# Performance work log

Measured on AMD Instinct MI355X. Metric: run time of the kernel, lower is better.

The kernel has to match this reference:

```python
import jax, jax.numpy as jnp
import numpy as np

EPS = 1e-10


def setup_inputs() -> dict:
    key = jax.random.key(0)
    k1, k2 = jax.random.split(key)
    x = jax.random.normal(k1, (64, 512, 256), dtype=jnp.float32)          # (N, code_dim, T)
    codebooks = jax.random.normal(k2, (6, 1024, 512), dtype=jnp.float32)  # (Q, nb_code, code_dim)
    return {"x": x, "codebooks": codebooks}


def _quantize_layer(x_flat, cb):
    # x_flat: (NT, D), cb: (C, D)
    dist = (jnp.sum(x_flat * x_flat, axis=-1, keepdims=True)
            - 2.0 * (x_flat @ cb.T)
            + jnp.sum(cb * cb, axis=-1))          # (NT, C)
    idx = jnp.argmin(dist, axis=-1)               # (NT,)
    x_d = cb[idx]                                 # gather, (NT, D)
    return idx, x_d


def reference(x, codebooks):
    N, D, T = x.shape
    Q, C, _ = codebooks.shape
    NT = N * T

    residual = x
    quantized_out = jnp.zeros_like(x)
    all_indices, losses, perps = [], [], []

    for q in range(Q):  # fixed small number of sequential quantizer stages
        cb = codebooks[q]
        # preprocess: (N, D, T) -> (NT, D)
        x_flat = residual.transpose(0, 2, 1).reshape(NT, D)
        idx, x_d = _quantize_layer(x_flat, cb)

        # commitment loss (codebook side detached; EMA-trained codebook)
        commit_loss = jnp.mean((x_flat - jax.lax.stop_gradient(x_d)) ** 2)

        # perplexity of code usage
        probs = jnp.zeros((C,), dtype=x.dtype).at[idx].add(1.0) / NT
        perplexity = jnp.exp(-jnp.sum(probs * jnp.log(probs + EPS)))

        # straight-through estimator, back to (N, D, T)
        quantized = x_flat + jax.lax.stop_gradient(x_d - x_flat)
        quantized = quantized.reshape(N, T, D).transpose(0, 2, 1)

        residual = residual - jax.lax.stop_gradient(quantized)
        quantized_out = quantized_out + quantized

        all_indices.append(idx.reshape(N, T))
        losses.append(commit_loss)
        perps.append(perplexity)

    all_indices = jnp.stack(all_indices, axis=-1)      # (N, T, Q)
    mean_loss = sum(losses) / Q
    mean_perplexity = sum(perps) / Q
    return quantized_out, all_indices, mean_loss, mean_perplexity
```

## Files before the change

### kernel.cpp

```cpp
#include <hip/hip_runtime.h>
#include <hip/hip_fp16.h>
#include <hip/hip_bf16.h>
#include <stdint.h>


#define NTROWS 16384
#define DDIM   512
#define CCODES 1024
#define QSTAGE 6

#define OFF_R      ((size_t)0)
#define OFF_RBF    ((size_t)33554432)
#define OFF_CBBF   ((size_t)50331648)
#define OFF_CAND   ((size_t)56623104)
#define OFF_CBSQ   ((size_t)58720256)
#define OFF_HIST   ((size_t)58744832)
#define OFF_LOSS   ((size_t)58769408)
#define WS_END     ((size_t)58775552)

#define OUT_IDX_OFF  ((size_t)8388608)
#define OUT_SCAL_OFF ((size_t)8486912)

typedef __attribute__((ext_vector_type(8))) short short8;
typedef __attribute__((ext_vector_type(8))) unsigned short ushort8v;
typedef __attribute__((ext_vector_type(4))) float f32x4;

__device__ __forceinline__ unsigned short f2bf(float f) {
    uint32_t u = __float_as_uint(f);
    uint32_t r = (u + 0x7fffu + ((u >> 16) & 1u)) >> 16;
    return (unsigned short)r;
}
__device__ __forceinline__ uint32_t fkey(float f) {
    uint32_t u = __float_as_uint(f);
    return u ^ ((uint32_t)((int32_t)u >> 31) | 0x80000000u);
}
__device__ __forceinline__ float funkey(uint32_t k) {
    uint32_t u = (k & 0x80000000u) ? (k ^ 0x80000000u) : ~k;
    return __uint_as_float(u);
}
__device__ __forceinline__ uint32_t umin32(uint32_t a, uint32_t b) { return a < b ? a : b; }
__device__ __forceinline__ uint32_t umax32(uint32_t a, uint32_t b) { return a > b ? a : b; }
__device__ __forceinline__ float wave_sum(float v) {
    for (int m = 32; m; m >>= 1) v += __shfl_xor(v, m, 64);
    return v;
}
__device__ __forceinline__ uint32_t wave_min_u32(uint32_t v) {
    for (int m = 32; m; m >>= 1) v = umin32(v, (uint32_t)__shfl_xor((int)v, m, 64));
    return v;
}
__device__ __forceinline__ void async_load16(const void* g, void* l) {
    __builtin_amdgcn_global_load_lds(
        (__attribute__((address_space(1))) void*)(void*)g,
        (__attribute__((address_space(3))) void*)l, 16, 0, 0);
}

__global__ __launch_bounds__(256) void prep_cb_kernel(
    const float* __restrict__ cb, unsigned short* __restrict__ cbbf,
    float* __restrict__ cbsq, unsigned int* __restrict__ hist,
    float* __restrict__ loss_bins)
{
    const int wave = threadIdx.x >> 6, lane = threadIdx.x & 63;
    const int row = blockIdx.x * 4 + wave;
    const float* p = cb + (size_t)row * DDIM;
    unsigned short* pb = cbbf + (size_t)row * DDIM;
    float s = 0.f;
#pragma unroll
    for (int t = 0; t < 8; ++t) {
        float v = p[lane + 64 * t];
        pb[lane + 64 * t] = f2bf(v);
        s += v * v;
    }
    s = wave_sum(s);
    if (lane == 0) cbsq[row] = s;
    if (blockIdx.x == 0) {
        for (int i = threadIdx.x; i < QSTAGE * CCODES; i += 256) hist[i] = 0u;
        for (int i = threadIdx.x; i < QSTAGE * 256; i += 256) loss_bins[i] = 0.f;
    }
}

__global__ void prep_x_kernel(const float* __restrict__ x, float* __restrict__ r,
                              unsigned short* __restrict__ rbf)
{
    __shared__ float tile[32][33];
    const int d0 = blockIdx.x * 32, t0 = blockIdx.y * 32, n = blockIdx.z;
    const int tx = threadIdx.x, ty = threadIdx.y;
    const float* xp = x + (size_t)n * (DDIM * 256);
#pragma unroll
    for (int s = 0; s < 4; ++s) {
        int dd = ty + s * 8;
        tile[dd][tx] = xp[(size_t)(d0 + dd) * 256 + t0 + tx];
    }
    __syncthreads();
#pragma unroll
    for (int s = 0; s < 4; ++s) {
        int tt = ty + s * 8;
        float v = tile[tx][tt];
        size_t off = (size_t)(n * 256 + t0 + tt) * DDIM + d0 + tx;
        r[off] = v;
        rbf[off] = f2bf(v);
    }
}

__global__ __launch_bounds__(256) void gemm_dist_kernel(
    const unsigned short* __restrict__ Abf,
    const unsigned short* __restrict__ Bbf,
    const float* __restrict__ cbsq,
    uint32_t* __restrict__ cand)
{
    __shared__ __align__(16) unsigned short lA[128 * 32];
    __shared__ __align__(16) unsigned short lB[128 * 32];
    const int tid = threadIdx.x;
    const int wave = tid >> 6, lane = tid & 63;
    const int quad = lane >> 4, l15 = lane & 15;
    const int tm = blockIdx.x, tn = blockIdx.y;
    const int wm = wave & 1, wn = wave >> 1;

    f32x4 acc[4][4];
#pragma unroll
    for (int i = 0; i < 4; ++i)
#pragma unroll
        for (int j = 0; j < 4; ++j) acc[i][j] = (f32x4){0.f, 0.f, 0.f, 0.f};

    const int srow = wave * 16 + (lane >> 2);
    const int gchunk = (lane & 3) ^ ((lane >> 3) & 3);
    const unsigned short* gA0 = Abf + (size_t)(tm * 128 + srow) * DDIM + gchunk * 8;
    const unsigned short* gA1 = gA0 + 64 * DDIM;
    const unsigned short* gB0 = Bbf + (size_t)(tn * 128 + srow) * DDIM + gchunk * 8;
    const unsigned short* gB1 = gB0 + 64 * DDIM;
    unsigned short* sA0 = &lA[srow * 32 + (lane & 3) * 8];
    unsigned short* sA1 = &lA[(64 + srow) * 32 + (lane & 3) * 8];
    unsigned short* sB0 = &lB[srow * 32 + (lane & 3) * 8];
    unsigned short* sB1 = &lB[(64 + srow) * 32 + (lane & 3) * 8];

    for (int kt = 0; kt < DDIM / 32; ++kt) {
        async_load16(gA0, sA0); async_load16(gA1, sA1);
        async_load16(gB0, sB0); async_load16(gB1, sB1);
        gA0 += 32; gA1 += 32; gB0 += 32; gB1 += 32;
        __syncthreads();
        short8 af[4], bfr[4];
        const int cqa = (quad ^ ((l15 >> 1) & 3)) * 8;
#pragma unroll
        for (int i = 0; i < 4; ++i)
            af[i] = *(const short8*)&lA[(wm * 64 + i * 16 + l15) * 32 + cqa];
#pragma unroll
        for (int j = 0; j < 4; ++j)
            bfr[j] = *(const short8*)&lB[(wn * 64 + j * 16 + l15) * 32 + cqa];
#pragma unroll
        for (int i = 0; i < 4; ++i)
#pragma unroll
            for (int j = 0; j < 4; ++j)
                acc[i][j] = __builtin_amdgcn_mfma_f32_16x16x32_bf16(
                    af[i], bfr[j], acc[i][j], 0, 0, 0);
        __syncthreads();
    }

    const int rowbase = tm * 128 + wm * 64 + quad * 4;
    const int colbase = tn * 128 + wn * 64 + l15;
    const int g = tn * 2 + wn;
    float cbs[4];
#pragma unroll
    for (int j = 0; j < 4; ++j) cbs[j] = cbsq[colbase + j * 16];
#pragma unroll
    for (int i = 0; i < 4; ++i) {
#pragma unroll
        for (int reg = 0; reg < 4; ++reg) {
            uint32_t k[4];
#pragma unroll
            for (int j = 0; j < 4; ++j) {
                float dv = cbs[j] - 2.0f * acc[i][j][reg];
                k[j] = (fkey(dv) & ~1023u) | (uint32_t)(colbase + j * 16);
            }
            uint32_t m01 = umin32(k[0], k[1]), M01 = umax32(k[0], k[1]);
            uint32_t m23 = umin32(k[2], k[3]), M23 = umax32(k[2], k[3]);
            uint32_t k1 = umin32(m01, m23);
            uint32_t k2 = umin32(umax32(m01, m23), umin32(M01, M23));
#pragma unroll
            for (int m = 1; m < 16; m <<= 1) {
                uint32_t o1 = (uint32_t)__shfl_xor((int)k1, m, 64);
                uint32_t o2 = (uint32_t)__shfl_xor((int)k2, m, 64);
                uint32_t n1 = umin32(k1, o1);
                uint32_t n2 = umin32(umax32(k1, o1), umin32(k2, o2));
                k1 = n1; k2 = n2;
            }
            if (l15 == 0) {
                const int row = rowbase + i * 16 + reg;
                *(uint2*)&cand[((size_t)row * 16 + g) * 2] = make_uint2(k1, k2);
            }
        }
    }
}

#define MARGIN 8.0f
__global__ __launch_bounds__(256) void refine_kernel(
    float* __restrict__ r, unsigned short* __restrict__ rbf,
    const float* __restrict__ cbq, const float* __restrict__ cbsqq,
    const uint32_t* __restrict__ cand,
    float* __restrict__ out_idx, unsigned int* __restrict__ histq,
    float* __restrict__ loss_bins, int q, int write_bf)
{
    const int wave = threadIdx.x >> 6, lane = threadIdx.x & 63;
    const int nt = blockIdx.x * 4 + wave;

    const float4* r4 = (const float4*)(r + (size_t)nt * DDIM);
    float4 ra = r4[lane * 2], rb = r4[lane * 2 + 1];
    float s = ra.x * ra.x + ra.y * ra.y + ra.z * ra.z + ra.w * ra.w
            + rb.x * rb.x + rb.y * rb.y + rb.z * rb.z + rb.w * rb.w;
    const float sumx = wave_sum(s);

    uint32_t key = 0xFFFFFFFFu;
    if (lane < 32) key = cand[(size_t)nt * 32 + lane];
    const uint32_t kmin = wave_min_u32(key);
    const float thr = funkey(kmin & ~1023u) + MARGIN;

    unsigned long long mask = __ballot(lane < 32 && funkey(key & ~1023u) <= thr);

    float best = 1e30f;
    int bestc = CCODES;
    while (mask) {
        const int src = __ffsll(mask) - 1;
        mask &= mask - 1;
        const int cc = __shfl((int)(key & 1023u), src, 64);
        const float4* crow = (const float4*)(cbq + (size_t)cc * DDIM);
        float4 ca = crow[lane * 2], cb2 = crow[lane * 2 + 1];
        float dot = ra.x * ca.x + ra.y * ca.y + ra.z * ca.z + ra.w * ca.w
                  + rb.x * cb2.x + rb.y * cb2.y + rb.z * cb2.z + rb.w * cb2.w;
        dot = wave_sum(dot);
        const float de = (sumx - 2.0f * dot) + cbsqq[cc];
        if (de < best || (de == best && cc < bestc)) { best = de; bestc = cc; }
    }

    const float4* cbest = (const float4*)(cbq + (size_t)bestc * DDIM);
    float4 ba = cbest[lane * 2], bb = cbest[lane * 2 + 1];
    float4 na = make_float4(ra.x - ba.x, ra.y - ba.y, ra.z - ba.z, ra.w - ba.w);
    float4 nb = make_float4(rb.x - bb.x, rb.y - bb.y, rb.z - bb.z, rb.w - bb.w);
    float4* rw = (float4*)(r + (size_t)nt * DDIM);
    rw[lane * 2] = na; rw[lane * 2 + 1] = nb;
    if (write_bf) {
        ushort8v pk;
        pk[0] = f2bf(na.x); pk[1] = f2bf(na.y); pk[2] = f2bf(na.z); pk[3] = f2bf(na.w);
        pk[4] = f2bf(nb.x); pk[5] = f2bf(nb.y); pk[6] = f2bf(nb.z); pk[7] = f2bf(nb.w);
        *(ushort8v*)(rbf + (size_t)nt * DDIM + lane * 8) = pk;
    }

    if (lane == 0) {
        out_idx[(size_t)nt * QSTAGE + q] = (float)bestc;
        atomicAdd(&histq[bestc], 1u);
        atomicAdd(&loss_bins[q * 256 + (blockIdx.x & 255)], best);
    }
}

__global__ void final_out_kernel(const float* __restrict__ x,
                                 const float* __restrict__ r,
                                 float* __restrict__ out)
{
    __shared__ float tile[32][33];
    const int d0 = blockIdx.x * 32, t0 = blockIdx.y * 32, n = blockIdx.z;
    const int tx = threadIdx.x, ty = threadIdx.y;
#pragma unroll
    for (int s = 0; s < 4; ++s) {
        int tt = ty + s * 8;
        tile[tt][tx] = r[(size_t)(n * 256 + t0 + tt) * DDIM + d0 + tx];
    }
    __syncthreads();
    const float* xp = x + (size_t)n * (DDIM * 256);
    float* op = out + (size_t)n * (DDIM * 256);
#pragma unroll
    for (int s = 0; s < 4; ++s) {
        int dd = ty + s * 8;
        size_t off = (size_t)(d0 + dd) * 256 + t0 + tx;
        op[off] = xp[off] - tile[tx][dd];
    }
}

__global__ __launch_bounds__(256) void scalars_kernel(
    const unsigned int* __restrict__ hist, const float* __restrict__ loss_bins,
    float* __restrict__ out2)
{
    __shared__ float red[4];
    __shared__ float perp_acc;
    const int tid = threadIdx.x, wave = tid >> 6, lane = tid & 63;
    if (tid == 0) perp_acc = 0.f;
    __syncthreads();
    for (int q = 0; q < QSTAGE; ++q) {
        float s = 0.f;
        for (int c = tid; c < CCODES; c += 256) {
            float p = (float)hist[q * CCODES + c] * (1.0f / (float)NTROWS);
            s += p * logf(p + 1e-10f);
        }
        s = wave_sum(s);
        if (lane == 0) red[wave] = s;
        __syncthreads();
        if (tid == 0) {
            float tot = red[0] + red[1] + red[2] + red[3];
            perp_acc += expf(-tot);
        }
        __syncthreads();
    }
    float ls = 0.f;
    for (int i = tid; i < QSTAGE * 256; i += 256) ls += loss_bins[i];
    ls = wave_sum(ls);
    if (lane == 0) red[wave] = ls;
    __syncthreads();
    if (tid == 0) {
        float lsum = red[0] + red[1] + red[2] + red[3];
        out2[0] = (lsum / (float)QSTAGE) / ((float)NTROWS * (float)DDIM);
        out2[1] = perp_acc / (float)QSTAGE;
    }
}

extern "C" void kernel_launch(void* const* d_in, const int* in_sizes, int n_in,
                              void* d_out, int out_size, void* d_ws, size_t ws_size,
                              hipStream_t stream)
{
    const float* x  = (const float*)d_in[0];
    const float* cb = (const float*)d_in[1];
    float* out = (float*)d_out;
    char* ws = (char*)d_ws;

    float*          r      = (float*)(ws + OFF_R);
    unsigned short* rbf    = (unsigned short*)(ws + OFF_RBF);
    unsigned short* cbbf   = (unsigned short*)(ws + OFF_CBBF);
    uint32_t*       cand   = (uint32_t*)(ws + OFF_CAND);
    float*          cbsq   = (float*)(ws + OFF_CBSQ);
    unsigned int*   hist   = (unsigned int*)(ws + OFF_HIST);
    float*          lbins  = (float*)(ws + OFF_LOSS);

    prep_cb_kernel<<<1536, 256, 0, stream>>>(cb, cbbf, cbsq, hist, lbins);
    prep_x_kernel<<<dim3(16, 8, 64), dim3(32, 8), 0, stream>>>(x, r, rbf);

    for (int q = 0; q < QSTAGE; ++q) {
        const size_t cboff = (size_t)q * CCODES * DDIM;
        gemm_dist_kernel<<<dim3(128, 8), 256, 0, stream>>>(
            rbf, cbbf + cboff, cbsq + q * CCODES, cand);
        refine_kernel<<<4096, 256, 0, stream>>>(
            r, rbf, cb + cboff, cbsq + q * CCODES, cand,
            out + OUT_IDX_OFF, hist + q * CCODES, lbins,
            q, (q < QSTAGE - 1) ? 1 : 0);
    }

    final_out_kernel<<<dim3(16, 8, 64), dim3(32, 8), 0, stream>>>(x, r, out);
    scalars_kernel<<<1, 256, 0, stream>>>(hist, lbins, out + OUT_SCAL_OFF);
}
```

Measured before the change: 503.6 us.

## Widen distance GEMM tile to 128x256 and merge prep and final launches

The distance GEMM now computes a 128x256 output tile per block, with 8 accumulator column fragments per wave. This halves the number of blocks and the number of times each residual tile is reloaded, and the candidate grouping is adjusted so each 64-column group still writes its top-2 keys. Separately, the two prep kernels are merged into one launch, as are the final output and scalar kernels, to cut launch overhead. The larger tile roughly doubles accumulator registers and LDS use and leaves only 512 blocks, which may hurt occupancy and load balance.

```diff
diff --git a/kernel.cpp b/kernel.cpp
--- a/kernel.cpp
+++ b/kernel.cpp
@@ -54,137 +54,148 @@
         (__attribute__((address_space(3))) void*)l, 16, 0, 0);
 }
 
-__global__ __launch_bounds__(256) void prep_cb_kernel(
-    const float* __restrict__ cb, unsigned short* __restrict__ cbbf,
-    float* __restrict__ cbsq, unsigned int* __restrict__ hist,
-    float* __restrict__ loss_bins)
-{
-    const int wave = threadIdx.x >> 6, lane = threadIdx.x & 63;
-    const int row = blockIdx.x * 4 + wave;
-    const float* p = cb + (size_t)row * DDIM;
-    unsigned short* pb = cbbf + (size_t)row * DDIM;
-    float s = 0.f;
-#pragma unroll
-    for (int t = 0; t < 8; ++t) {
-        float v = p[lane + 64 * t];
-        pb[lane + 64 * t] = f2bf(v);
-        s += v * v;
-    }
-    s = wave_sum(s);
-    if (lane == 0) cbsq[row] = s;
-    if (blockIdx.x == 0) {
-        for (int i = threadIdx.x; i < QSTAGE * CCODES; i += 256) hist[i] = 0u;
-        for (int i = threadIdx.x; i < QSTAGE * 256; i += 256) loss_bins[i] = 0.f;
-    }
-}
-
-__global__ void prep_x_kernel(const float* __restrict__ x, float* __restrict__ r,
-                              unsigned short* __restrict__ rbf)
+__global__ __launch_bounds__(256) void prep_kernel(
+    const float* __restrict__ x, const float* __restrict__ cb,
+    float* __restrict__ r, unsigned short* __restrict__ rbf,
+    unsigned short* __restrict__ cbbf, float* __restrict__ cbsq,
+    unsigned int* __restrict__ hist, float* __restrict__ loss_bins)
 {
     __shared__ float tile[32][33];
-    const int d0 = blockIdx.x * 32, t0 = blockIdx.y * 32, n = blockIdx.z;
-    const int tx = threadIdx.x, ty = threadIdx.y;
-    const float* xp = x + (size_t)n * (DDIM * 256);
-#pragma unroll
-    for (int s = 0; s < 4; ++s) {
-        int dd = ty + s * 8;
-        tile[dd][tx] = xp[(size_t)(d0 + dd) * 256 + t0 + tx];
-    }
-    __syncthreads();
-#pragma unroll
-    for (int s = 0; s < 4; ++s) {
-        int tt = ty + s * 8;
-        float v = tile[tx][tt];
-        size_t off = (size_t)(n * 256 + t0 + tt) * DDIM + d0 + tx;
-        r[off] = v;
-        rbf[off] = f2bf(v);
-    }
-}
-
-__global__ __launch_bounds__(256) void gemm_dist_kernel(
+    if (blockIdx.x < 1536) {
+        const int wave = threadIdx.x >> 6, lane = threadIdx.x & 63;
+        const int row = blockIdx.x * 4 + wave;
+        const float* p = cb + (size_t)row * DDIM;
+        unsigned short* pb = cbbf + (size_t)row * DDIM;
+        float s = 0.f;
+#pragma unroll
+        for (int t = 0; t < 8; ++t) {
+            float v = p[lane + 64 * t];
+            pb[lane + 64 * t] = f2bf(v);
+            s += v * v;
+        }
+        s = wave_sum(s);
+        if (lane == 0) cbsq[row] = s;
+        if (blockIdx.x == 0) {
+            for (int i = threadIdx.x; i < QSTAGE * CCODES; i += 256) hist[i] = 0u;
+            for (int i = threadIdx.x; i < QSTAGE * 256; i += 256) loss_bins[i] = 0.f;
+        }
+    } else {
+        const int bidx = blockIdx.x - 1536;
+        const int d0 = (bidx & 15) * 32;
+        const int t0 = ((bidx >> 4) & 7) * 32;
+        const int n  = bidx >> 7;
+        const int tx = threadIdx.x & 31, ty = threadIdx.x >> 5;
+        const float* xp = x + (size_t)n * (DDIM * 256);
+#pragma unroll
+        for (int s = 0; s < 4; ++s) {
+            int dd = ty + s * 8;
+            tile[dd][tx] = xp[(size_t)(d0 + dd) * 256 + t0 + tx];
+        }
+        __syncthreads();
+#pragma unroll
+        for (int s = 0; s < 4; ++s) {
+            int tt = ty + s * 8;
+            float v = tile[tx][tt];
+            size_t off = (size_t)(n * 256 + t0 + tt) * DDIM + d0 + tx;
+            r[off] = v;
+            rbf[off] = f2bf(v);
+        }
+    }
+}
+
+__global__ __launch_bounds__(256, 2) void gemm_dist_kernel(
     const unsigned short* __restrict__ Abf,
     const unsigned short* __restrict__ Bbf,
     const float* __restrict__ cbsq,
     uint32_t* __restrict__ cand)
 {
     __shared__ __align__(16) unsigned short lA[128 * 32];
-    __shared__ __align__(16) unsigned short lB[128 * 32];
+    __shared__ __align__(16) unsigned short lB[256 * 32];
     const int tid = threadIdx.x;
     const int wave = tid >> 6, lane = tid & 63;
     const int quad = lane >> 4, l15 = lane & 15;
-    const int tm = blockIdx.x, tn = blockIdx.y;
+    const int tm = blockIdx.x, tn2 = blockIdx.y;
     const int wm = wave & 1, wn = wave >> 1;
 
-    f32x4 acc[4][4];
+    f32x4 acc[4][8];
 #pragma unroll
     for (int i = 0; i < 4; ++i)
 #pragma unroll
-        for (int j = 0; j < 4; ++j) acc[i][j] = (f32x4){0.f, 0.f, 0.f, 0.f};
+        for (int j = 0; j < 8; ++j) acc[i][j] = (f32x4){0.f, 0.f, 0.f, 0.f};
 
     const int srow = wave * 16 + (lane >> 2);
     const int gchunk = (lane & 3) ^ ((lane >> 3) & 3);
     const unsigned short* gA0 = Abf + (size_t)(tm * 128 + srow) * DDIM + gchunk * 8;
     const unsigned short* gA1 = gA0 + 64 * DDIM;
-    const unsigned short* gB0 = Bbf + (size_t)(tn * 128 + srow) * DDIM + gchunk * 8;
+    const unsigned short* gB0 = Bbf + (size_t)(tn2 * 256 + srow) * DDIM + gchunk * 8;
     const unsigned short* gB1 = gB0 + 64 * DDIM;
+    const unsigned short* gB2 = gB0 + 128 * DDIM;
+    const unsigned short* gB3 = gB0 + 192 * DDIM;
     unsigned short* sA0 = &lA[srow * 32 + (lane & 3) * 8];
     unsigned short* sA1 = &lA[(64 + srow) * 32 + (lane & 3) * 8];
     unsigned short* sB0 = &lB[srow * 32 + (lane & 3) * 8];
     unsigned short* sB1 = &lB[(64 + srow) * 32 + (lane & 3) * 8];
+    unsigned short* sB2 = &lB[(128 + srow) * 32 + (lane & 3) * 8];
+    unsigned short* sB3 = &lB[(192 + srow) * 32 + (lane & 3) * 8];
 
     for (int kt = 0; kt < DDIM / 32; ++kt) {
         async_load16(gA0, sA0); async_load16(gA1, sA1);
         async_load16(gB0, sB0); async_load16(gB1, sB1);
-        gA0 += 32; gA1 += 32; gB0 += 32; gB1 += 32;
-        __syncthreads();
-        short8 af[4], bfr[4];
+        async_load16(gB2, sB2); async_load16(gB3, sB3);
+        gA0 += 32; gA1 += 32; gB0 += 32; gB1 += 32; gB2 += 32; gB3 += 32;
+        __syncthreads();
         const int cqa = (quad ^ ((l15 >> 1) & 3)) * 8;
+        short8 af[4], bfr[8];
 #pragma unroll
         for (int i = 0; i < 4; ++i)
             af[i] = *(const short8*)&lA[(wm * 64 + i * 16 + l15) * 32 + cqa];
 #pragma unroll
-        for (int j = 0; j < 4; ++j)
-            bfr[j] = *(const short8*)&lB[(wn * 64 + j * 16 + l15) * 32 + cqa];
+        for (int j = 0; j < 8; ++j)
+            bfr[j] = *(const short8*)&lB[(wn * 128 + j * 16 + l15) * 32 + cqa];
 #pragma unroll
         for (int i = 0; i < 4; ++i)
 #pragma unroll
-            for (int j = 0; j < 4; ++j)
+            for (int j = 0; j < 8; ++j)
                 acc[i][j] = __builtin_amdgcn_mfma_f32_16x16x32_bf16(
                     af[i], bfr[j], acc[i][j], 0, 0, 0);
         __syncthreads();
     }
 
     const int rowbase = tm * 128 + wm * 64 + quad * 4;
-    const int colbase = tn * 128 + wn * 64 + l15;
-    const int g = tn * 2 + wn;
-    float cbs[4];
-#pragma unroll
-    for (int j = 0; j < 4; ++j) cbs[j] = cbsq[colbase + j * 16];
+    const int colbase = tn2 * 256 + wn * 128 + l15;
+    const int gbase = tn2 * 4 + wn * 2;
+    float cbs[8];
+#pragma unroll
+    for (int j = 0; j < 8; ++j) cbs[j] = cbsq[colbase + j * 16];
 #pragma unroll
     for (int i = 0; i < 4; ++i) {
 #pragma unroll
         for (int reg = 0; reg < 4; ++reg) {
-            uint32_t k[4];
-#pragma unroll
-            for (int j = 0; j < 4; ++j) {
-                float dv = cbs[j] - 2.0f * acc[i][j][reg];
-                k[j] = (fkey(dv) & ~1023u) | (uint32_t)(colbase + j * 16);
-            }
-            uint32_t m01 = umin32(k[0], k[1]), M01 = umax32(k[0], k[1]);
-            uint32_t m23 = umin32(k[2], k[3]), M23 = umax32(k[2], k[3]);
-            uint32_t k1 = umin32(m01, m23);
-            uint32_t k2 = umin32(umax32(m01, m23), umin32(M01, M23));
-#pragma unroll
-            for (int m = 1; m < 16; m <<= 1) {
-                uint32_t o1 = (uint32_t)__shfl_xor((int)k1, m, 64);
-                uint32_t o2 = (uint32_t)__shfl_xor((int)k2, m, 64);
-                uint32_t n1 = umin32(k1, o1);
-                uint32_t n2 = umin32(umax32(k1, o1), umin32(k2, o2));
-                k1 = n1; k2 = n2;
-            }
-            if (l15 == 0) {
-                const int row = rowbase + i * 16 + reg;
-                *(uint2*)&cand[((size_t)row * 16 + g) * 2] = make_uint2(k1, k2);
+            const int row = rowbase + i * 16 + reg;
+#pragma unroll
+            for (int jh = 0; jh < 2; ++jh) {
+                uint32_t k[4];
+#pragma unroll
+                for (int jj = 0; jj < 4; ++jj) {
+                    const int j = jh * 4 + jj;
+                    float dv = cbs[j] - 2.0f * acc[i][j][reg];
+                    k[jj] = (fkey(dv) & ~1023u) | (uint32_t)(colbase + j * 16);
+                }
+                uint32_t m01 = umin32(k[0], k[1]), M01 = umax32(k[0], k[1]);
+                uint32_t m23 = umin32(k[2], k[3]), M23 = umax32(k[2], k[3]);
+                uint32_t k1 = umin32(m01, m23);
+                uint32_t k2 = umin32(umax32(m01, m23), umin32(M01, M23));
+#pragma unroll
+                for (int m = 1; m < 16; m <<= 1) {
+                    uint32_t o1 = (uint32_t)__shfl_xor((int)k1, m, 64);
+                    uint32_t o2 = (uint32_t)__shfl_xor((int)k2, m, 64);
+                    uint32_t n1 = umin32(k1, o1);
+                    uint32_t n2 = umin32(umax32(k1, o1), umin32(k2, o2));
+                    k1 = n1; k2 = n2;
+                }
+                if (l15 == 0)
+                    *(uint2*)&cand[((size_t)row * 16 + gbase + jh) * 2] =
+                        make_uint2(k1, k2);
             }
         }
     }
@@ -249,36 +260,40 @@
     }
 }
 
-__global__ void final_out_kernel(const float* __restrict__ x,
-                                 const float* __restrict__ r,
-                                 float* __restrict__ out)
-{
-    __shared__ float tile[32][33];
-    const int d0 = blockIdx.x * 32, t0 = blockIdx.y * 32, n = blockIdx.z;
-    const int tx = threadIdx.x, ty = threadIdx.y;
-#pragma unroll
-    for (int s = 0; s < 4; ++s) {
-        int tt = ty + s * 8;
-        tile[tt][tx] = r[(size_t)(n * 256 + t0 + tt) * DDIM + d0 + tx];
-    }
-    __syncthreads();
-    const float* xp = x + (size_t)n * (DDIM * 256);
-    float* op = out + (size_t)n * (DDIM * 256);
-#pragma unroll
-    for (int s = 0; s < 4; ++s) {
-        int dd = ty + s * 8;
-        size_t off = (size_t)(d0 + dd) * 256 + t0 + tx;
-        op[off] = xp[off] - tile[tx][dd];
-    }
-}
-
-__global__ __launch_bounds__(256) void scalars_kernel(
+__global__ __launch_bounds__(256) void final_kernel(
+    const float* __restrict__ x, const float* __restrict__ r,
+    float* __restrict__ out,
     const unsigned int* __restrict__ hist, const float* __restrict__ loss_bins,
     float* __restrict__ out2)
 {
+    __shared__ float tile[32][33];
     __shared__ float red[4];
     __shared__ float perp_acc;
     const int tid = threadIdx.x, wave = tid >> 6, lane = tid & 63;
+
+    if (blockIdx.x < 8192) {
+        const int bidx = blockIdx.x;
+        const int d0 = (bidx & 15) * 32;
+        const int t0 = ((bidx >> 4) & 7) * 32;
+        const int n  = bidx >> 7;
+        const int tx = tid & 31, ty = tid >> 5;
+#pragma unroll
+        for (int s = 0; s < 4; ++s) {
+            int tt = ty + s * 8;
+            tile[tt][tx] = r[(size_t)(n * 256 + t0 + tt) * DDIM + d0 + tx];
+        }
+        __syncthreads();
+        const float* xp = x + (size_t)n * (DDIM * 256);
+        float* op = out + (size_t)n * (DDIM * 256);
+#pragma unroll
+        for (int s = 0; s < 4; ++s) {
+            int dd = ty + s * 8;
+            size_t off = (size_t)(d0 + dd) * 256 + t0 + tx;
+            op[off] = xp[off] - tile[tx][dd];
+        }
+        return;
+    }
+
     if (tid == 0) perp_acc = 0.f;
     __syncthreads();
     for (int q = 0; q < QSTAGE; ++q) {
@@ -325,12 +340,11 @@
     unsigned int*   hist   = (unsigned int*)(ws + OFF_HIST);
     float*          lbins  = (float*)(ws + OFF_LOSS);
 
-    prep_cb_kernel<<<1536, 256, 0, stream>>>(cb, cbbf, cbsq, hist, lbins);
-    prep_x_kernel<<<dim3(16, 8, 64), dim3(32, 8), 0, stream>>>(x, r, rbf);
+    prep_kernel<<<9728, 256, 0, stream>>>(x, cb, r, rbf, cbbf, cbsq, hist, lbins);
 
     for (int q = 0; q < QSTAGE; ++q) {
         const size_t cboff = (size_t)q * CCODES * DDIM;
-        gemm_dist_kernel<<<dim3(128, 8), 256, 0, stream>>>(
+        gemm_dist_kernel<<<dim3(128, 4), 256, 0, stream>>>(
             rbf, cbbf + cboff, cbsq + q * CCODES, cand);
         refine_kernel<<<4096, 256, 0, stream>>>(
             r, rbf, cb + cboff, cbsq + q * CCODES, cand,
@@ -338,6 +352,6 @@
             q, (q < QSTAGE - 1) ? 1 : 0);
     }
 
-    final_out_kernel<<<dim3(16, 8, 64), dim3(32, 8), 0, stream>>>(x, r, out);
-    scalars_kernel<<<1, 256, 0, stream>>>(hist, lbins, out + OUT_SCAL_OFF);
-}
+    final_kernel<<<8193, 256, 0, stream>>>(x, r, out, hist, lbins,
+                                           out + OUT_SCAL_OFF);
+}
```

New measurement: 476.0 us. 5.5% less time.
